# Kernel optimization log

Measured on AMD Instinct MI355X. Metric: run time of the kernel, lower is better.

Reference implementation:

```python
import jax, jax.numpy as jnp
import numpy as np

N_NETS = 10  # classNum
DIMS = [784, 128, 64, 12, 3, 12, 64, 128, 784]  # encoder 784->3, decoder 3->784
BATCH = 8192


def setup_inputs() -> dict:
    key = jax.random.key(0)
    keys = jax.random.split(key, 1 + 2 * 8)
    inp = {"x": jax.random.normal(keys[0], (BATCH, DIMS[0]), dtype=jnp.float32)}
    for l in range(8):
        scale = 1.0 / np.sqrt(DIMS[l]).astype(np.float32)
        inp[f"W{l}"] = jax.random.normal(keys[1 + 2 * l], (N_NETS, DIMS[l], DIMS[l + 1]), dtype=jnp.float32) * scale
        inp[f"b{l}"] = jax.random.normal(keys[2 + 2 * l], (N_NETS, DIMS[l + 1]), dtype=jnp.float32) * 0.01
    return inp


def reference(x, W0, b0, W1, b1, W2, b2, W3, b3, W4, b4, W5, b5, W6, b6, W7, b7):
    Ws = [W0, W1, W2, W3, W4, W5, W6, W7]
    bs = [b0, b1, b2, b3, b4, b5, b6, b7]
    # layer 0: broadcast x over the 10 nets -> [B, N, 128]
    h = jnp.einsum('bi,nio->bno', x, Ws[0]) + bs[0]
    h = jax.nn.relu(h)
    for l in range(1, 8):
        h = jnp.einsum('bni,nio->bno', h, Ws[l]) + bs[l]
        if l in (1, 2, 4, 5, 6):      # hidden ReLUs (layer 3 = latent, no act)
            h = jax.nn.relu(h)
        elif l == 7:                  # decoder output Tanh
            h = jnp.tanh(h)
    # outputSum[i, net] = sum of net's reconstruction of x[i]
    return jnp.sum(h, axis=-1)  # [B, 10]
```

## Files before the change

kernel.cpp:

```cpp
#include <hip/hip_runtime.h>

#define NNETS 10
#define BATCH 8192

typedef __attribute__((ext_vector_type(8)))  short  short8;
typedef __attribute__((ext_vector_type(16))) float  f32x16;

#define XPACK_BYTES  (256UL*49*64*8*2)
#define W0PACK_OFF   (XPACK_BYTES)
#define W0PACK_BYTES (10UL*49*4*2*64*8*2)
#define W7PACK_OFF   (W0PACK_OFF + W0PACK_BYTES)
#define W7PACK_BYTES (10UL*8*25*2*64*8*2)
#define W1PACK_OFF   (W7PACK_OFF + W7PACK_BYTES)
#define W1PACK_BYTES (10UL*8*2*2*64*8*2)
#define W6PACK_OFF   (W1PACK_OFF + W1PACK_BYTES)
#define W6PACK_BYTES (10UL*4*4*2*64*8*2)
#define TOTAL_WS     (W6PACK_OFF + W6PACK_BYTES)

#define PX_BLOCKS  (256 * 7)
#define PW0_BLOCKS 490
#define PW7_BLOCKS 500
#define PW1_BLOCKS 40
#define PW6_BLOCKS 40
#define PACK_GRID  (PX_BLOCKS + PW0_BLOCKS + PW7_BLOCKS + PW1_BLOCKS + PW6_BLOCKS)

__device__ __forceinline__ float fast_tanh(float x) {
    float e = __expf(2.f * x);
    return 1.f - 2.f / (1.f + e);
}
__device__ __forceinline__ unsigned short bf16_rne(float v) {
    unsigned u = __float_as_uint(v);
    unsigned r = (u + 0x7FFFu + ((u >> 16) & 1u)) >> 16;
    return (unsigned short)r;
}
__device__ __forceinline__ float bf16_to_f(unsigned short h) {
    return __uint_as_float(((unsigned)h) << 16);
}
__device__ __forceinline__ unsigned split_pack(float v) {
    unsigned short h = bf16_rne(v);
    unsigned short l = bf16_rne(v - bf16_to_f(h));
    return (unsigned)h | ((unsigned)l << 16);
}

__device__ __forceinline__ void pack_x_body(int blk, int t, const float* __restrict__ x,
                                            unsigned short* __restrict__ xp,
                                            float (*xs)[113]) {
    const int rt = blk / 7;
    const int c  = blk - rt * 7;
#pragma unroll
    for (int it = 0; it < 4; ++it) {
        int f = t + 256 * it;
        if (f < 896) {
            int row  = f / 28;
            int colq = f - row * 28;
            float4 v = *(const float4*)(x + (size_t)(rt * 32 + row) * 784 + c * 112 + colq * 4);
            xs[row][colq * 4 + 0] = v.x;
            xs[row][colq * 4 + 1] = v.y;
            xs[row][colq * 4 + 2] = v.z;
            xs[row][colq * 4 + 3] = v.w;
        }
    }
    __syncthreads();
    const int lane = t & 63;
    const int sub  = t >> 6;
    const int srow = lane & 31;
    const int skb  = 8 * (lane >> 5);
    for (int kcl = sub; kcl < 7; kcl += 4) {
        short8 V;
#pragma unroll
        for (int j = 0; j < 8; ++j)
            V[j] = (short)bf16_rne(xs[srow][kcl * 16 + skb + j]);
        int kc_global = c * 7 + kcl;
        short8* dst = reinterpret_cast<short8*>(xp) + (size_t)(rt * 49 + kc_global) * 64 + lane;
        *dst = V;
    }
}

__device__ __forceinline__ void pack_w0_body(int tid, const float* __restrict__ W0,
                                             unsigned short* __restrict__ wp) {
    if (tid >= 10 * 49 * 4 * 64) return;
    int lane = tid & 63; int t2 = tid >> 6;
    int ct = t2 % 4;  t2 /= 4;
    int kc = t2 % 49; int n = t2 / 49;
    int col = ct * 32 + (lane & 31);
    int kb  = kc * 16 + 8 * (lane >> 5);
    short8 H, L;
#pragma unroll
    for (int j = 0; j < 8; ++j) {
        float v = W0[((size_t)n * 784 + kb + j) * 128 + col];
        unsigned short h = bf16_rne(v);
        H[j] = (short)h;
        L[j] = (short)bf16_rne(v - bf16_to_f(h));
    }
    short8* dst = reinterpret_cast<short8*>(wp + (size_t)((n * 49 + kc) * 4 + ct) * 1024) + lane;
    dst[0]  = H;
    dst[64] = L;
}

__device__ __forceinline__ void pack_w7_body(int tid, const float* __restrict__ W7,
                                             unsigned short* __restrict__ wp) {
    if (tid >= 10 * 8 * 25 * 64) return;
    int lane = tid & 63; int t2 = tid >> 6;
    int ct = t2 % 25; t2 /= 25;
    int kc = t2 % 8;  int n = t2 / 8;
    int col = ct * 32 + (lane & 31);
    int kb  = kc * 16 + 8 * (lane >> 5);
    short8 H, L;
#pragma unroll
    for (int j = 0; j < 8; ++j) {
        float v = (col < 784) ? W7[((size_t)n * 128 + kb + j) * 784 + col] : 0.f;
        unsigned short h = bf16_rne(v);
        H[j] = (short)h;
        L[j] = (short)bf16_rne(v - bf16_to_f(h));
    }
    short8* dst = reinterpret_cast<short8*>(wp + (size_t)((n * 8 + kc) * 25 + ct) * 1024) + lane;
    dst[0]  = H;
    dst[64] = L;
}

__device__ __forceinline__ void pack_w1_body(int tid, const float* __restrict__ W1,
                                             unsigned short* __restrict__ wp) {
    if (tid >= 10 * 8 * 2 * 64) return;
    int lane = tid & 63; int t2 = tid >> 6;
    int ct = t2 % 2; t2 /= 2;
    int kc = t2 % 8; int n = t2 / 8;
    int col = ct * 32 + (lane & 31);
    int kb  = kc * 16 + 8 * (lane >> 5);
    short8 H, L;
#pragma unroll
    for (int j = 0; j < 8; ++j) {
        float v = W1[((size_t)n * 128 + kb + j) * 64 + col];
        unsigned short h = bf16_rne(v);
        H[j] = (short)h;
        L[j] = (short)bf16_rne(v - bf16_to_f(h));
    }
    short8* dst = reinterpret_cast<short8*>(wp + (size_t)((n * 8 + kc) * 2 + ct) * 1024) + lane;
    dst[0]  = H;
    dst[64] = L;
}

__device__ __forceinline__ void pack_w6_body(int tid, const float* __restrict__ W6,
                                             unsigned short* __restrict__ wp) {
    if (tid >= 10 * 4 * 4 * 64) return;
    int lane = tid & 63; int t2 = tid >> 6;
    int ct = t2 % 4; t2 /= 4;
    int kc = t2 % 4; int n = t2 / 4;
    int col = ct * 32 + (lane & 31);
    int kb  = kc * 16 + 8 * (lane >> 5);
    short8 H, L;
#pragma unroll
    for (int j = 0; j < 8; ++j) {
        float v = W6[((size_t)n * 64 + kb + j) * 128 + col];
        unsigned short h = bf16_rne(v);
        H[j] = (short)h;
        L[j] = (short)bf16_rne(v - bf16_to_f(h));
    }
    short8* dst = reinterpret_cast<short8*>(wp + (size_t)((n * 4 + kc) * 4 + ct) * 1024) + lane;
    dst[0]  = H;
    dst[64] = L;
}

__global__ __launch_bounds__(256)
void pack_all_kernel(const float* __restrict__ x,
                     const float* __restrict__ W0, const float* __restrict__ W1,
                     const float* __restrict__ W6, const float* __restrict__ W7,
                     unsigned short* __restrict__ ws_u16) {
    __shared__ float xs[32][113];
    int b = blockIdx.x;
    if (b < PX_BLOCKS) {
        pack_x_body(b, threadIdx.x, x, ws_u16, xs);
    } else if (b < PX_BLOCKS + PW0_BLOCKS) {
        pack_w0_body((b - PX_BLOCKS) * 256 + threadIdx.x, W0, ws_u16 + W0PACK_OFF / 2);
    } else if (b < PX_BLOCKS + PW0_BLOCKS + PW7_BLOCKS) {
        pack_w7_body((b - PX_BLOCKS - PW0_BLOCKS) * 256 + threadIdx.x, W7, ws_u16 + W7PACK_OFF / 2);
    } else if (b < PX_BLOCKS + PW0_BLOCKS + PW7_BLOCKS + PW1_BLOCKS) {
        pack_w1_body((b - PX_BLOCKS - PW0_BLOCKS - PW7_BLOCKS) * 256 + threadIdx.x, W1, ws_u16 + W1PACK_OFF / 2);
    } else {
        pack_w6_body((b - PX_BLOCKS - PW0_BLOCKS - PW7_BLOCKS - PW1_BLOCKS) * 256 + threadIdx.x, W6, ws_u16 + W6PACK_OFF / 2);
    }
}

template<int ID, int OD, int NO, bool RELU>
__device__ __forceinline__ void midlayer(const float* __restrict__ W,
                                         const float* __restrict__ bias,
                                         const float* bufIn, float* bufOut,
                                         int n, int w, int lane) {
    const int o0 = w * NO;
    if (o0 < OD) {
        float acc[NO];
#pragma unroll
        for (int j = 0; j < NO; ++j) acc[j] = bias[n * OD + o0 + j];
        for (int k = 0; k < ID; ++k) {
            float a = bufIn[k * 65 + lane];
            const float* Wk = W + ((size_t)n * ID + k) * OD + o0;
#pragma unroll
            for (int j = 0; j < NO; ++j) acc[j] = fmaf(a, Wk[j], acc[j]);
        }
#pragma unroll
        for (int j = 0; j < NO; ++j) {
            float v = acc[j];
            if (RELU) v = fmaxf(v, 0.f);
            bufOut[(o0 + j) * 65 + lane] = v;
        }
    }
    __syncthreads();
}

#define MFMA32(A, B, C) __builtin_amdgcn_mfma_f32_32x32x16_bf16(A, B, C, 0, 0, 0)

__global__ __launch_bounds__(256)
void fused_ae_mfma_kernel(const float* __restrict__ B0,
                          const float* __restrict__ B1,
                          const float* __restrict__ W2, const float* __restrict__ B2,
                          const float* __restrict__ W3, const float* __restrict__ B3,
                          const float* __restrict__ W4, const float* __restrict__ B4,
                          const float* __restrict__ W5, const float* __restrict__ B5,
                          const float* __restrict__ B6,
                          const float* __restrict__ B7,
                          const unsigned short* __restrict__ ws_u16,
                          float* __restrict__ out) {
    __shared__ float HsA[128 * 65];
    __shared__ float HsB[64 * 65];
    unsigned* HsAu = reinterpret_cast<unsigned*>(HsA);

    const int t    = threadIdx.x;
    const int lane = t & 63;
    const int w    = __builtin_amdgcn_readfirstlane(t >> 6);

    const int bid = blockIdx.x;
    const int g   = bid & 7;
    const int j8  = bid >> 3;
    const int yb  = (g << 4) + (j8 / 10);
    const int n   = j8 % 10;

    const int cl   = lane & 31;
    const int hf   = lane >> 5;
    const int rtl  = w >> 1;
    const int ct0  = (w & 1) * 2;

    const short8* xp8  = reinterpret_cast<const short8*>(ws_u16);
    const short8* w0p8 = reinterpret_cast<const short8*>(ws_u16 + W0PACK_OFF / 2);
    const short8* w7p8 = reinterpret_cast<const short8*>(ws_u16 + W7PACK_OFF / 2);
    const short8* w1p8 = reinterpret_cast<const short8*>(ws_u16 + W1PACK_OFF / 2);
    const short8* w6p8 = reinterpret_cast<const short8*>(ws_u16 + W6PACK_OFF / 2);

    const int rt = yb * 2 + rtl;
    f32x16 acc0, acc1;
#pragma unroll
    for (int i = 0; i < 16; ++i) { acc0[i] = 0.f; acc1[i] = 0.f; }

    const short8* xA = xp8 + (size_t)rt * 49 * 64 + lane;
    const short8* wB = w0p8 + ((size_t)n * 49 * 4 + ct0) * 128 + lane;

    short8 Ah = xA[0];
    short8 Bh0 = wB[0], Bl0 = wB[64], Bh1 = wB[128], Bl1 = wB[192];
    for (int kc = 0; kc < 49; ++kc) {
        short8 nAh, nBh0, nBl0, nBh1, nBl1;
        if (kc < 48) {
            const short8* xn = xA + (size_t)(kc + 1) * 64;
            const short8* wn = wB + (size_t)(kc + 1) * 512;
            nAh = xn[0];
            nBh0 = wn[0]; nBl0 = wn[64]; nBh1 = wn[128]; nBl1 = wn[192];
        }
        acc0 = MFMA32(Ah, Bh0, acc0);
        acc0 = MFMA32(Ah, Bl0, acc0);
        acc1 = MFMA32(Ah, Bh1, acc1);
        acc1 = MFMA32(Ah, Bl1, acc1);
        if (kc < 48) { Ah = nAh; Bh0 = nBh0; Bl0 = nBl0; Bh1 = nBh1; Bl1 = nBl1; }
    }
    {
        float b0a = B0[n * 128 + ct0 * 32 + cl];
        float b0b = B0[n * 128 + (ct0 + 1) * 32 + cl];
#pragma unroll
        for (int r2 = 0; r2 < 16; ++r2) {
            int row = rtl * 32 + (r2 & 3) + 8 * (r2 >> 2) + 4 * hf;
            HsAu[(ct0 * 32 + cl) * 65 + row]       = split_pack(fmaxf(acc0[r2] + b0a, 0.f));
            HsAu[((ct0 + 1) * 32 + cl) * 65 + row] = split_pack(fmaxf(acc1[r2] + b0b, 0.f));
        }
    }
    __syncthreads();

    {
        const int ctl = w & 1;
        short8 a_hi[8], a_lo[8];
        const int r32 = rtl * 32 + cl;
#pragma unroll
        for (int kc = 0; kc < 8; ++kc) {
            int kb = kc * 16 + 8 * hf;
            short8 H, L;
#pragma unroll
            for (int j = 0; j < 8; ++j) {
                unsigned u = HsAu[(kb + j) * 65 + r32];
                H[j] = (short)(u & 0xFFFFu);
                L[j] = (short)(u >> 16);
            }
            a_hi[kc] = H; a_lo[kc] = L;
        }
        f32x16 acc;
#pragma unroll
        for (int i = 0; i < 16; ++i) acc[i] = 0.f;
        const short8* wb = w1p8 + ((size_t)n * 16 + ctl) * 128 + lane;
#pragma unroll
        for (int kc = 0; kc < 8; ++kc) {
            const short8* bp = wb + (size_t)kc * 256;
            short8 Bh = bp[0], Bl = bp[64];
            acc = MFMA32(a_hi[kc], Bh, acc);
            acc = MFMA32(a_hi[kc], Bl, acc);
            acc = MFMA32(a_lo[kc], Bh, acc);
        }
        __syncthreads();
        float bias = B1[n * 64 + ctl * 32 + cl];
#pragma unroll
        for (int r2 = 0; r2 < 16; ++r2) {
            int row = rtl * 32 + (r2 & 3) + 8 * (r2 >> 2) + 4 * hf;
            HsB[(ctl * 32 + cl) * 65 + row] = fmaxf(acc[r2] + bias, 0.f);
        }
    }
    __syncthreads();

    midlayer< 64, 12,  3, true >(W2, B2, HsB, HsA, n, w, lane);
    midlayer< 12,  3,  1, false>(W3, B3, HsA, HsB, n, w, lane);
    midlayer<  3, 12,  3, true >(W4, B4, HsB, HsA, n, w, lane);
    midlayer< 12, 64, 16, true >(W5, B5, HsA, HsB, n, w, lane);

    {
        short8 a_hi[4], a_lo[4];
        const int r32 = rtl * 32 + cl;
#pragma unroll
        for (int kc = 0; kc < 4; ++kc) {
            int kb = kc * 16 + 8 * hf;
            short8 H, L;
#pragma unroll
            for (int j = 0; j < 8; ++j) {
                float v = HsB[(kb + j) * 65 + r32];
                unsigned short h = bf16_rne(v);
                H[j] = (short)h;
                L[j] = (short)bf16_rne(v - bf16_to_f(h));
            }
            a_hi[kc] = H; a_lo[kc] = L;
        }
        f32x16 acc0b, acc1b;
#pragma unroll
        for (int i = 0; i < 16; ++i) { acc0b[i] = 0.f; acc1b[i] = 0.f; }
        const short8* wb = w6p8 + ((size_t)n * 16 + ct0) * 128 + lane;
#pragma unroll
        for (int kc = 0; kc < 4; ++kc) {
            const short8* bp = wb + (size_t)kc * 512;
            short8 Bh0 = bp[0],   Bl0 = bp[64];
            short8 Bh1 = bp[128], Bl1 = bp[192];
            acc0b = MFMA32(a_hi[kc], Bh0, acc0b);
            acc0b = MFMA32(a_hi[kc], Bl0, acc0b);
            acc0b = MFMA32(a_lo[kc], Bh0, acc0b);
            acc1b = MFMA32(a_hi[kc], Bh1, acc1b);
            acc1b = MFMA32(a_hi[kc], Bl1, acc1b);
            acc1b = MFMA32(a_lo[kc], Bh1, acc1b);
        }
        __syncthreads();
        float b6a = B6[n * 128 + ct0 * 32 + cl];
        float b6b = B6[n * 128 + (ct0 + 1) * 32 + cl];
#pragma unroll
        for (int r2 = 0; r2 < 16; ++r2) {
            int row = rtl * 32 + (r2 & 3) + 8 * (r2 >> 2) + 4 * hf;
            HsAu[(ct0 * 32 + cl) * 65 + row]       = split_pack(fmaxf(acc0b[r2] + b6a, 0.f));
            HsAu[((ct0 + 1) * 32 + cl) * 65 + row] = split_pack(fmaxf(acc1b[r2] + b6b, 0.f));
        }
    }
    __syncthreads();

    short8 a_hi[8], a_lo[8];
    {
        const int r32 = rtl * 32 + cl;
#pragma unroll
        for (int kc = 0; kc < 8; ++kc) {
            int kb = kc * 16 + 8 * hf;
            short8 H, L;
#pragma unroll
            for (int j = 0; j < 8; ++j) {
                unsigned u = HsAu[(kb + j) * 65 + r32];
                H[j] = (short)(u & 0xFFFFu);
                L[j] = (short)(u >> 16);
            }
            a_hi[kc] = H; a_lo[kc] = L;
        }
    }

    float rowsum[16];
#pragma unroll
    for (int i = 0; i < 16; ++i) rowsum[i] = 0.f;

    const short8* w7b = w7p8 + (size_t)n * 8 * 25 * 128 + lane;
    const int ctS = (w & 1) ? 13 : 0;
    const int ctE = (w & 1) ? 25 : 13;
    for (int ct = ctS; ct < ctE; ++ct) {
        f32x16 acc;
#pragma unroll
        for (int i = 0; i < 16; ++i) acc[i] = 0.f;
#pragma unroll
        for (int kc = 0; kc < 8; ++kc) {
            const short8* bp = w7b + (size_t)(kc * 25 + ct) * 128;
            short8 Bh = bp[0], Bl = bp[64];
            acc = MFMA32(a_hi[kc], Bh, acc);
            acc = MFMA32(a_hi[kc], Bl, acc);
            acc = MFMA32(a_lo[kc], Bh, acc);
        }
        int col = ct * 32 + cl;
        if (col < 784) {
            float bias = B7[n * 784 + col];
#pragma unroll
            for (int r2 = 0; r2 < 16; ++r2) rowsum[r2] += fast_tanh(acc[r2] + bias);
        }
    }

#pragma unroll
    for (int r2 = 0; r2 < 16; ++r2) {
        float s = rowsum[r2];
        s += __shfl_xor(s, 1);  s += __shfl_xor(s, 2);  s += __shfl_xor(s, 4);
        s += __shfl_xor(s, 8);  s += __shfl_xor(s, 16);
        rowsum[r2] = s;
    }

    float* Ps = HsB;
    Ps[t] = 0.f;
    __syncthreads();
    if (cl == 0) {
#pragma unroll
        for (int r2 = 0; r2 < 16; ++r2) {
            int row = rtl * 32 + (r2 & 3) + 8 * (r2 >> 2) + 4 * hf;
            Ps[w * 64 + row] = rowsum[r2];
        }
    }
    __syncthreads();
    if (t < 64) {
        float s = Ps[t] + Ps[64 + t] + Ps[128 + t] + Ps[192 + t];
        out[(size_t)(yb * 64 + t) * 10 + n] = s;
    }
}

__global__ __launch_bounds__(256)
void fused_ae_fp32_kernel(const float* __restrict__ x,
                          const float* __restrict__ W0, const float* __restrict__ B0,
                          const float* __restrict__ W1, const float* __restrict__ B1,
                          const float* __restrict__ W2, const float* __restrict__ B2,
                          const float* __restrict__ W3, const float* __restrict__ B3,
                          const float* __restrict__ W4, const float* __restrict__ B4,
                          const float* __restrict__ W5, const float* __restrict__ B5,
                          const float* __restrict__ W6, const float* __restrict__ B6,
                          const float* __restrict__ W7, const float* __restrict__ B7,
                          float* __restrict__ out) {
    __shared__ float HsA[128 * 65];
    __shared__ float HsB[64 * 65];
    const int t    = threadIdx.x;
    const int lane = t & 63;
    const int w    = __builtin_amdgcn_readfirstlane(t >> 6);
    const int n    = blockIdx.x;
    const int rowbase = blockIdx.y * 64;

    float acc0[32];
#pragma unroll
    for (int j = 0; j < 32; ++j) acc0[j] = 0.f;
    float* As = HsB;
    const int r   = t >> 2;
    const int kk4 = (t & 3) * 4;
    const float* xrow = x + (size_t)(rowbase + r) * 784;
    for (int kc = 0; kc < 49; ++kc) {
        float4 xv = *(const float4*)(xrow + kc * 16 + kk4);
        As[(kk4 + 0) * 65 + r] = xv.x;
        As[(kk4 + 1) * 65 + r] = xv.y;
        As[(kk4 + 2) * 65 + r] = xv.z;
        As[(kk4 + 3) * 65 + r] = xv.w;
        __syncthreads();
        const float* W0base = W0 + ((size_t)n * 784 + (size_t)kc * 16) * 128 + w * 32;
#pragma unroll
        for (int k = 0; k < 16; ++k) {
            float a = As[k * 65 + lane];
            const float* Wk = W0base + k * 128;
#pragma unroll
            for (int j = 0; j < 32; ++j) acc0[j] = fmaf(a, Wk[j], acc0[j]);
        }
        __syncthreads();
    }
    {
        const float* bb = B0 + n * 128 + w * 32;
#pragma unroll
        for (int j = 0; j < 32; ++j)
            HsA[(w * 32 + j) * 65 + lane] = fmaxf(acc0[j] + bb[j], 0.f);
    }
    __syncthreads();

    midlayer<128, 64, 16, true >(W1, B1, HsA, HsB, n, w, lane);
    midlayer< 64, 12,  3, true >(W2, B2, HsB, HsA, n, w, lane);
    midlayer< 12,  3,  1, false>(W3, B3, HsA, HsB, n, w, lane);
    midlayer<  3, 12,  3, true >(W4, B4, HsB, HsA, n, w, lane);
    midlayer< 12, 64, 16, true >(W5, B5, HsA, HsB, n, w, lane);
    midlayer< 64,128, 32, true >(W6, B6, HsB, HsA, n, w, lane);

    float lane_sum = 0.f;
    const int j0w = w * 196;
    for (int c = 0; c < 7; ++c) {
        const int j0 = j0w + c * 28;
        float acc[28];
        const float* bb = B7 + n * 784 + j0;
#pragma unroll
        for (int j = 0; j < 28; ++j) acc[j] = bb[j];
        for (int k = 0; k < 128; ++k) {
            float a = HsA[k * 65 + lane];
            const float* Wk = W7 + ((size_t)n * 128 + k) * 784 + j0;
#pragma unroll
            for (int j = 0; j < 28; ++j) acc[j] = fmaf(a, Wk[j], acc[j]);
        }
#pragma unroll
        for (int j = 0; j < 28; ++j) lane_sum += fast_tanh(acc[j]);
    }
    float* partial = HsB;
    partial[w * 64 + lane] = lane_sum;
    __syncthreads();
    if (t < 64) {
        float s = partial[t] + partial[64 + t] + partial[128 + t] + partial[192 + t];
        out[(size_t)(rowbase + t) * 10 + n] = s;
    }
}

extern "C" void kernel_launch(void* const* d_in, const int* in_sizes, int n_in,
                              void* d_out, int out_size, void* d_ws, size_t ws_size,
                              hipStream_t stream) {
    (void)in_sizes; (void)n_in; (void)out_size;
    const float* x  = (const float*)d_in[0];
    const float* W0 = (const float*)d_in[1];  const float* B0 = (const float*)d_in[2];
    const float* W1 = (const float*)d_in[3];  const float* B1 = (const float*)d_in[4];
    const float* W2 = (const float*)d_in[5];  const float* B2 = (const float*)d_in[6];
    const float* W3 = (const float*)d_in[7];  const float* B3 = (const float*)d_in[8];
    const float* W4 = (const float*)d_in[9];  const float* B4 = (const float*)d_in[10];
    const float* W5 = (const float*)d_in[11]; const float* B5 = (const float*)d_in[12];
    const float* W6 = (const float*)d_in[13]; const float* B6 = (const float*)d_in[14];
    const float* W7 = (const float*)d_in[15]; const float* B7 = (const float*)d_in[16];
    float* out = (float*)d_out;

    if (ws_size >= TOTAL_WS) {
        unsigned short* ws_u16 = (unsigned short*)d_ws;
        hipLaunchKernelGGL(pack_all_kernel, dim3(PACK_GRID), dim3(256), 0, stream,
                           x, W0, W1, W6, W7, ws_u16);
        hipLaunchKernelGGL(fused_ae_mfma_kernel, dim3(NNETS * (BATCH / 64)), dim3(256), 0, stream,
                           B0, B1, W2, B2, W3, B3, W4, B4, W5, B5, B6, B7, ws_u16, out);
    } else {
        hipLaunchKernelGGL(fused_ae_fp32_kernel, dim3(NNETS, BATCH / 64), dim3(256), 0, stream,
                           x, W0, B0, W1, B1, W2, B2, W3, B3,
                           W4, B4, W5, B5, W6, B6, W7, B7, out);
    }
}
```

Before: 258.6 us.

## Convert x to bf16 inside fused kernel instead of separate pack pass

Removes the x pre-packing stage from the pack kernel and has the fused MFMA kernel load fp32 x rows directly with float4 loads, converting them to bf16 in registers. This drops a full write and reread of the packed x buffer but makes each of the 10 per-net blocks reread fp32 x (twice the bytes of bf16) with a less MFMA-friendly access pattern. It also splits the layer-7 MFMA chain across two accumulators to shorten dependency stalls, and replaces the tanh division with a hardware reciprocal.

```diff
diff --git a/kernel.cpp b/kernel.cpp
--- a/kernel.cpp
+++ b/kernel.cpp
@@ -1,4 +1,5 @@
 #include <hip/hip_runtime.h>
+#include <hip/hip_bf16.h>
 
 #define NNETS 10
 #define BATCH 8192
@@ -6,8 +7,7 @@
 typedef __attribute__((ext_vector_type(8)))  short  short8;
 typedef __attribute__((ext_vector_type(16))) float  f32x16;
 
-#define XPACK_BYTES  (256UL*49*64*8*2)
-#define W0PACK_OFF   (XPACK_BYTES)
+#define W0PACK_OFF   0UL
 #define W0PACK_BYTES (10UL*49*4*2*64*8*2)
 #define W7PACK_OFF   (W0PACK_OFF + W0PACK_BYTES)
 #define W7PACK_BYTES (10UL*8*25*2*64*8*2)
@@ -17,16 +17,15 @@
 #define W6PACK_BYTES (10UL*4*4*2*64*8*2)
 #define TOTAL_WS     (W6PACK_OFF + W6PACK_BYTES)
 
-#define PX_BLOCKS  (256 * 7)
 #define PW0_BLOCKS 490
 #define PW7_BLOCKS 500
 #define PW1_BLOCKS 40
 #define PW6_BLOCKS 40
-#define PACK_GRID  (PX_BLOCKS + PW0_BLOCKS + PW7_BLOCKS + PW1_BLOCKS + PW6_BLOCKS)
+#define PACK_GRID  (PW0_BLOCKS + PW7_BLOCKS + PW1_BLOCKS + PW6_BLOCKS)
 
 __device__ __forceinline__ float fast_tanh(float x) {
     float e = __expf(2.f * x);
-    return 1.f - 2.f / (1.f + e);
+    return 1.f - 2.f * __builtin_amdgcn_rcpf(1.f + e);
 }
 __device__ __forceinline__ unsigned short bf16_rne(float v) {
     unsigned u = __float_as_uint(v);
@@ -41,39 +40,15 @@
     unsigned short l = bf16_rne(v - bf16_to_f(h));
     return (unsigned)h | ((unsigned)l << 16);
 }
-
-__device__ __forceinline__ void pack_x_body(int blk, int t, const float* __restrict__ x,
-                                            unsigned short* __restrict__ xp,
-                                            float (*xs)[113]) {
-    const int rt = blk / 7;
-    const int c  = blk - rt * 7;
-#pragma unroll
-    for (int it = 0; it < 4; ++it) {
-        int f = t + 256 * it;
-        if (f < 896) {
-            int row  = f / 28;
-            int colq = f - row * 28;
-            float4 v = *(const float4*)(x + (size_t)(rt * 32 + row) * 784 + c * 112 + colq * 4);
-            xs[row][colq * 4 + 0] = v.x;
-            xs[row][colq * 4 + 1] = v.y;
-            xs[row][colq * 4 + 2] = v.z;
-            xs[row][colq * 4 + 3] = v.w;
-        }
-    }
-    __syncthreads();
-    const int lane = t & 63;
-    const int sub  = t >> 6;
-    const int srow = lane & 31;
-    const int skb  = 8 * (lane >> 5);
-    for (int kcl = sub; kcl < 7; kcl += 4) {
-        short8 V;
-#pragma unroll
-        for (int j = 0; j < 8; ++j)
-            V[j] = (short)bf16_rne(xs[srow][kcl * 16 + skb + j]);
-        int kc_global = c * 7 + kcl;
-        short8* dst = reinterpret_cast<short8*>(xp) + (size_t)(rt * 49 + kc_global) * 64 + lane;
-        *dst = V;
-    }
+__device__ __forceinline__ short f2bf(float v) {
+    __hip_bfloat16 b = __float2bfloat16(v);
+    return *reinterpret_cast<short*>(&b);
+}
+__device__ __forceinline__ short8 cvt8(float4 a, float4 b) {
+    short8 r;
+    r[0] = f2bf(a.x); r[1] = f2bf(a.y); r[2] = f2bf(a.z); r[3] = f2bf(a.w);
+    r[4] = f2bf(b.x); r[5] = f2bf(b.y); r[6] = f2bf(b.z); r[7] = f2bf(b.w);
+    return r;
 }
 
 __device__ __forceinline__ void pack_w0_body(int tid, const float* __restrict__ W0,
@@ -161,22 +136,18 @@
 }
 
 __global__ __launch_bounds__(256)
-void pack_all_kernel(const float* __restrict__ x,
-                     const float* __restrict__ W0, const float* __restrict__ W1,
+void pack_all_kernel(const float* __restrict__ W0, const float* __restrict__ W1,
                      const float* __restrict__ W6, const float* __restrict__ W7,
                      unsigned short* __restrict__ ws_u16) {
-    __shared__ float xs[32][113];
     int b = blockIdx.x;
-    if (b < PX_BLOCKS) {
-        pack_x_body(b, threadIdx.x, x, ws_u16, xs);
-    } else if (b < PX_BLOCKS + PW0_BLOCKS) {
-        pack_w0_body((b - PX_BLOCKS) * 256 + threadIdx.x, W0, ws_u16 + W0PACK_OFF / 2);
-    } else if (b < PX_BLOCKS + PW0_BLOCKS + PW7_BLOCKS) {
-        pack_w7_body((b - PX_BLOCKS - PW0_BLOCKS) * 256 + threadIdx.x, W7, ws_u16 + W7PACK_OFF / 2);
-    } else if (b < PX_BLOCKS + PW0_BLOCKS + PW7_BLOCKS + PW1_BLOCKS) {
-        pack_w1_body((b - PX_BLOCKS - PW0_BLOCKS - PW7_BLOCKS) * 256 + threadIdx.x, W1, ws_u16 + W1PACK_OFF / 2);
+    if (b < PW0_BLOCKS) {
+        pack_w0_body(b * 256 + threadIdx.x, W0, ws_u16 + W0PACK_OFF / 2);
+    } else if (b < PW0_BLOCKS + PW7_BLOCKS) {
+        pack_w7_body((b - PW0_BLOCKS) * 256 + threadIdx.x, W7, ws_u16 + W7PACK_OFF / 2);
+    } else if (b < PW0_BLOCKS + PW7_BLOCKS + PW1_BLOCKS) {
+        pack_w1_body((b - PW0_BLOCKS - PW7_BLOCKS) * 256 + threadIdx.x, W1, ws_u16 + W1PACK_OFF / 2);
     } else {
-        pack_w6_body((b - PX_BLOCKS - PW0_BLOCKS - PW7_BLOCKS - PW1_BLOCKS) * 256 + threadIdx.x, W6, ws_u16 + W6PACK_OFF / 2);
+        pack_w6_body((b - PW0_BLOCKS - PW7_BLOCKS - PW1_BLOCKS) * 256 + threadIdx.x, W6, ws_u16 + W6PACK_OFF / 2);
     }
 }
 
@@ -209,7 +180,8 @@
 #define MFMA32(A, B, C) __builtin_amdgcn_mfma_f32_32x32x16_bf16(A, B, C, 0, 0, 0)
 
 __global__ __launch_bounds__(256)
-void fused_ae_mfma_kernel(const float* __restrict__ B0,
+void fused_ae_mfma_kernel(const float* __restrict__ x,
+                          const float* __restrict__ B0,
                           const float* __restrict__ B1,
                           const float* __restrict__ W2, const float* __restrict__ B2,
                           const float* __restrict__ W3, const float* __restrict__ B3,
@@ -238,7 +210,6 @@
     const int rtl  = w >> 1;
     const int ct0  = (w & 1) * 2;
 
-    const short8* xp8  = reinterpret_cast<const short8*>(ws_u16);
     const short8* w0p8 = reinterpret_cast<const short8*>(ws_u16 + W0PACK_OFF / 2);
     const short8* w7p8 = reinterpret_cast<const short8*>(ws_u16 + W7PACK_OFF / 2);
     const short8* w1p8 = reinterpret_cast<const short8*>(ws_u16 + W1PACK_OFF / 2);
@@ -249,17 +220,20 @@
 #pragma unroll
     for (int i = 0; i < 16; ++i) { acc0[i] = 0.f; acc1[i] = 0.f; }
 
-    const short8* xA = xp8 + (size_t)rt * 49 * 64 + lane;
+    const float* xrow = x + (size_t)(rt * 32 + cl) * 784 + 8 * hf;
     const short8* wB = w0p8 + ((size_t)n * 49 * 4 + ct0) * 128 + lane;
 
-    short8 Ah = xA[0];
+    float4 xv0 = *(const float4*)(xrow);
+    float4 xv1 = *(const float4*)(xrow + 4);
+    short8 Ah = cvt8(xv0, xv1);
     short8 Bh0 = wB[0], Bl0 = wB[64], Bh1 = wB[128], Bl1 = wB[192];
     for (int kc = 0; kc < 49; ++kc) {
         short8 nAh, nBh0, nBl0, nBh1, nBl1;
         if (kc < 48) {
-            const short8* xn = xA + (size_t)(kc + 1) * 64;
+            float4 nv0 = *(const float4*)(xrow + (kc + 1) * 16);
+            float4 nv1 = *(const float4*)(xrow + (kc + 1) * 16 + 4);
+            nAh = cvt8(nv0, nv1);
             const short8* wn = wB + (size_t)(kc + 1) * 512;
-            nAh = xn[0];
             nBh0 = wn[0]; nBl0 = wn[64]; nBh1 = wn[128]; nBl1 = wn[192];
         }
         acc0 = MFMA32(Ah, Bh0, acc0);
@@ -392,22 +366,23 @@
     const int ctS = (w & 1) ? 13 : 0;
     const int ctE = (w & 1) ? 25 : 13;
     for (int ct = ctS; ct < ctE; ++ct) {
-        f32x16 acc;
-#pragma unroll
-        for (int i = 0; i < 16; ++i) acc[i] = 0.f;
+        f32x16 accA, accB;
+#pragma unroll
+        for (int i = 0; i < 16; ++i) { accA[i] = 0.f; accB[i] = 0.f; }
 #pragma unroll
         for (int kc = 0; kc < 8; ++kc) {
             const short8* bp = w7b + (size_t)(kc * 25 + ct) * 128;
             short8 Bh = bp[0], Bl = bp[64];
-            acc = MFMA32(a_hi[kc], Bh, acc);
-            acc = MFMA32(a_hi[kc], Bl, acc);
-            acc = MFMA32(a_lo[kc], Bh, acc);
+            accA = MFMA32(a_hi[kc], Bh, accA);
+            accB = MFMA32(a_hi[kc], Bl, accB);
+            accA = MFMA32(a_lo[kc], Bh, accA);
         }
         int col = ct * 32 + cl;
         if (col < 784) {
             float bias = B7[n * 784 + col];
 #pragma unroll
-            for (int r2 = 0; r2 < 16; ++r2) rowsum[r2] += fast_tanh(acc[r2] + bias);
+            for (int r2 = 0; r2 < 16; ++r2)
+                rowsum[r2] += fast_tanh(accA[r2] + accB[r2] + bias);
         }
     }
 
@@ -538,9 +513,9 @@
     if (ws_size >= TOTAL_WS) {
         unsigned short* ws_u16 = (unsigned short*)d_ws;
         hipLaunchKernelGGL(pack_all_kernel, dim3(PACK_GRID), dim3(256), 0, stream,
-                           x, W0, W1, W6, W7, ws_u16);
+                           W0, W1, W6, W7, ws_u16);
         hipLaunchKernelGGL(fused_ae_mfma_kernel, dim3(NNETS * (BATCH / 64)), dim3(256), 0, stream,
-                           B0, B1, W2, B2, W3, B3, W4, B4, W5, B5, B6, B7, ws_u16, out);
+                           x, B0, B1, W2, B2, W3, B3, W4, B4, W5, B5, B6, B7, ws_u16, out);
     } else {
         hipLaunchKernelGGL(fused_ae_fp32_kernel, dim3(NNETS, BATCH / 64), dim3(256), 0, stream,
                            x, W0, B0, W1, B1, W2, B2, W3, B3,
```

After: 277.7 us. +7.4%, slower.

## Add split-bf16 low part for x in layer 0 and split W7 accumulator chain

Applied to the files above, without the earlier changes.

The packed input x now stores a bf16 hi/lo pair, and layer 0 adds a third MFMA (x_lo * W_hi) per k-chunk. This raises accuracy but doubles x pack traffic and adds 50% more layer-0 MFMAs. The layer-7 MFMA chain is split across two accumulators to cut the dependency chain length. tanh now uses a hardware reciprocal instead of a division.

```diff
diff --git a/kernel.cpp b/kernel.cpp
--- a/kernel.cpp
+++ b/kernel.cpp
@@ -6,7 +6,7 @@
 typedef __attribute__((ext_vector_type(8)))  short  short8;
 typedef __attribute__((ext_vector_type(16))) float  f32x16;
 
-#define XPACK_BYTES  (256UL*49*64*8*2)
+#define XPACK_BYTES  (256UL*49*2*64*8*2)
 #define W0PACK_OFF   (XPACK_BYTES)
 #define W0PACK_BYTES (10UL*49*4*2*64*8*2)
 #define W7PACK_OFF   (W0PACK_OFF + W0PACK_BYTES)
@@ -26,7 +26,7 @@
 
 __device__ __forceinline__ float fast_tanh(float x) {
     float e = __expf(2.f * x);
-    return 1.f - 2.f / (1.f + e);
+    return 1.f - 2.f * __builtin_amdgcn_rcpf(1.f + e);
 }
 __device__ __forceinline__ unsigned short bf16_rne(float v) {
     unsigned u = __float_as_uint(v);
@@ -65,13 +65,19 @@
     const int sub  = t >> 6;
     const int srow = lane & 31;
     const int skb  = 8 * (lane >> 5);
-    for (int kcl = sub; kcl < 7; kcl += 4) {
+    for (int idx = sub; idx < 14; idx += 4) {
+        int kcl = idx >> 1;
+        int hl  = idx & 1;
         short8 V;
 #pragma unroll
-        for (int j = 0; j < 8; ++j)
-            V[j] = (short)bf16_rne(xs[srow][kcl * 16 + skb + j]);
+        for (int j = 0; j < 8; ++j) {
+            float v = xs[srow][kcl * 16 + skb + j];
+            unsigned short h = bf16_rne(v);
+            if (hl == 0) V[j] = (short)h;
+            else         V[j] = (short)bf16_rne(v - bf16_to_f(h));
+        }
         int kc_global = c * 7 + kcl;
-        short8* dst = reinterpret_cast<short8*>(xp) + (size_t)(rt * 49 + kc_global) * 64 + lane;
+        short8* dst = reinterpret_cast<short8*>(xp) + (size_t)(rt * 49 + kc_global) * 128 + hl * 64 + lane;
         *dst = V;
     }
 }
@@ -249,24 +255,26 @@
 #pragma unroll
     for (int i = 0; i < 16; ++i) { acc0[i] = 0.f; acc1[i] = 0.f; }
 
-    const short8* xA = xp8 + (size_t)rt * 49 * 64 + lane;
+    const short8* xA = xp8 + (size_t)rt * 49 * 128 + lane;
     const short8* wB = w0p8 + ((size_t)n * 49 * 4 + ct0) * 128 + lane;
 
-    short8 Ah = xA[0];
+    short8 Ah = xA[0], Al = xA[64];
     short8 Bh0 = wB[0], Bl0 = wB[64], Bh1 = wB[128], Bl1 = wB[192];
     for (int kc = 0; kc < 49; ++kc) {
-        short8 nAh, nBh0, nBl0, nBh1, nBl1;
+        short8 nAh, nAl, nBh0, nBl0, nBh1, nBl1;
         if (kc < 48) {
-            const short8* xn = xA + (size_t)(kc + 1) * 64;
+            const short8* xn = xA + (size_t)(kc + 1) * 128;
             const short8* wn = wB + (size_t)(kc + 1) * 512;
-            nAh = xn[0];
+            nAh = xn[0]; nAl = xn[64];
             nBh0 = wn[0]; nBl0 = wn[64]; nBh1 = wn[128]; nBl1 = wn[192];
         }
         acc0 = MFMA32(Ah, Bh0, acc0);
         acc0 = MFMA32(Ah, Bl0, acc0);
+        acc0 = MFMA32(Al, Bh0, acc0);
         acc1 = MFMA32(Ah, Bh1, acc1);
         acc1 = MFMA32(Ah, Bl1, acc1);
-        if (kc < 48) { Ah = nAh; Bh0 = nBh0; Bl0 = nBl0; Bh1 = nBh1; Bl1 = nBl1; }
+        acc1 = MFMA32(Al, Bh1, acc1);
+        if (kc < 48) { Ah = nAh; Al = nAl; Bh0 = nBh0; Bl0 = nBl0; Bh1 = nBh1; Bl1 = nBl1; }
     }
     {
         float b0a = B0[n * 128 + ct0 * 32 + cl];
@@ -392,22 +400,23 @@
     const int ctS = (w & 1) ? 13 : 0;
     const int ctE = (w & 1) ? 25 : 13;
     for (int ct = ctS; ct < ctE; ++ct) {
-        f32x16 acc;
-#pragma unroll
-        for (int i = 0; i < 16; ++i) acc[i] = 0.f;
+        f32x16 accA, accB;
+#pragma unroll
+        for (int i = 0; i < 16; ++i) { accA[i] = 0.f; accB[i] = 0.f; }
 #pragma unroll
         for (int kc = 0; kc < 8; ++kc) {
             const short8* bp = w7b + (size_t)(kc * 25 + ct) * 128;
             short8 Bh = bp[0], Bl = bp[64];
-            acc = MFMA32(a_hi[kc], Bh, acc);
-            acc = MFMA32(a_hi[kc], Bl, acc);
-            acc = MFMA32(a_lo[kc], Bh, acc);
+            accA = MFMA32(a_hi[kc], Bh, accA);
+            accB = MFMA32(a_hi[kc], Bl, accB);
+            accA = MFMA32(a_lo[kc], Bh, accA);
         }
         int col = ct * 32 + cl;
         if (col < 784) {
             float bias = B7[n * 784 + col];
 #pragma unroll
-            for (int r2 = 0; r2 < 16; ++r2) rowsum[r2] += fast_tanh(acc[r2] + bias);
+            for (int r2 = 0; r2 < 16; ++r2)
+                rowsum[r2] += fast_tanh(accA[r2] + accB[r2] + bias);
         }
     }
 
```

Measured after the change: 277.5 us. 7.3% more time.
